# Optimization experiments

Measured on AMD Instinct MI355X. Metric: run time of the kernel, lower is better.

## Reference

```python
import jax, jax.numpy as jnp
import numpy as np

EPS = 1e-12  # tf.nn.l2_normalize epsilon used inside keras CosineSimilarity


def _cos(a, b):
    # keras CosineSimilarity returns -cos; callers negate explicitly.
    an = a / jnp.sqrt(jnp.maximum(jnp.sum(a * a, axis=-1, keepdims=True), EPS))
    bn = b / jnp.sqrt(jnp.maximum(jnp.sum(b * b, axis=-1, keepdims=True), EPS))
    return jnp.sum(an * bn, axis=-1)


def setup_inputs() -> dict:
    key = jax.random.key(0)
    B, S, D, H, N = 1024, 200, 128, 128, 64
    ks = jax.random.split(key, 8)
    X_series = jax.random.normal(ks[0], (B, S, D), jnp.float32)
    pos_series = jax.random.normal(ks[1], (S, D), jnp.float32)
    X_item = jax.random.normal(ks[2], (B, D), jnp.float32)
    origin = jax.random.normal(ks[3], (B, N, D), jnp.float32)  # X_negative
    # contiguous-prefix validity mask (module assumes valid positions form a prefix)
    lengths = jax.random.randint(ks[4], (B,), 1, S + 1)
    valid_mask = jnp.arange(S)[None, :] < lengths[:, None]
    # learned params (GlorotUniform-scale init)
    Wp = jax.random.normal(ks[5], (D, H), jnp.float32) * 0.08
    We = jax.random.normal(ks[6], (D, H), jnp.float32) * 0.08
    z = jax.random.normal(ks[7], (H,), jnp.float32) * 0.1
    return {"X_series": X_series, "pos_series": pos_series, "X_item": X_item,
            "valid_mask": valid_mask, "origin": origin, "Wp": Wp, "We": We, "z": z}


def reference(X_series, pos_series, X_item, valid_mask, origin, Wp, We, z):
    B, S, D = X_series.shape
    # additive tanh attention: z . tanh(X_series @ We + pos_series @ Wp)
    hidden = jnp.tanh(jnp.einsum('bsd,dh->bsh', X_series, We) + (pos_series @ Wp)[None])
    scores = jnp.einsum('bsh,h->bs', hidden, z)
    scores = jnp.where(valid_mask, scores, -jnp.inf)
    attn = jax.nn.softmax(scores, axis=-1)                      # [B,S]
    attentioned = attn[:, :, None] * X_series                    # [B,S,D]
    attention_output = jnp.sum(attentioned, axis=1)              # [B,D]
    inner = jnp.sum(attention_output * X_item, axis=-1, keepdims=True)
    concated = jnp.concatenate([attention_output, inner], axis=1)  # [B,D+1]

    # ---- auxiliary loss ----
    last_idx = jnp.sum(valid_mask.astype(jnp.int32), axis=1) - 1
    last_vec = attentioned[jnp.arange(B), last_idx]              # gather_nd
    new_mask = (jnp.arange(S)[None, :] < last_idx[:, None]).astype(X_series.dtype)
    out_vec = jnp.sum(attentioned * new_mask[:, :, None], axis=1)  # [B,D]
    # keras CosineSimilarity = -cos_sim; then mapped to (x+1)/2 and used as logits
    pos_logits = (-_cos(last_vec, out_vec) + 1.0) / 2.0          # [B]
    neg_logits = (-_cos(origin, out_vec[:, None, :]) + 1.0) / 2.0  # [B,N]
    pos_loss = jax.nn.softplus(-pos_logits)  # sigmoid_xent labels=1
    neg_loss = jax.nn.softplus(neg_logits)   # sigmoid_xent labels=0
    # NB: TF reduces pos_loss over its only axis -> scalar, broadcast-added to [B]
    auxiliary_loss = jnp.sum(pos_loss) + jnp.sum(neg_loss, axis=-1)  # [B]
    return concated, auxiliary_loss
```

## Files before the change

kernel.cpp:

```cpp
#include <hip/hip_runtime.h>
#include <hip/hip_bf16.h>
#include <math.h>

#define B_ 1024
#define S_ 200
#define D_ 128
#define H_ 128
#define N_ 64

typedef __attribute__((ext_vector_type(8))) short short8;
typedef __attribute__((ext_vector_type(8))) __bf16 bf16x8;
typedef __attribute__((ext_vector_type(4))) float floatx4;

static __device__ __forceinline__ float bf2f(unsigned short u) {
    union { unsigned int i; float f; } v; v.i = ((unsigned int)u) << 16; return v.f;
}
static __device__ __forceinline__ unsigned short f2bf(float f) {
    union { float f; unsigned int u; } v; v.f = f;
    unsigned int u = v.u;
    return (unsigned short)((u + 0x7FFFu + ((u >> 16) & 1u)) >> 16);
}
static __device__ __forceinline__ float ld1(const void* p, int isbf, size_t i) {
    return isbf ? bf2f(((const unsigned short*)p)[i]) : ((const float*)p)[i];
}
static __device__ __forceinline__ float fast_tanh(float x) {
    float t = __expf(2.0f * x);
    return 1.0f - 2.0f * __builtin_amdgcn_rcpf(t + 1.0f);
}

__global__ __launch_bounds__(64) void detect_kernel(
    const void* a0, const void* a1, const void* a2, const void* a3,
    const void* a4, const void* a5, const void* a6, const void* a7,
    int* flags)
{
    int bid = blockIdx.x, t = threadIdx.x;
    if (bid == 3) {
        const unsigned char* mb = (const unsigned char*)a3;
        int f = 0;
        for (int i = t; i < 4096; i += 64)
            if ((i & 3) && mb[i]) f = 1;
        for (int off = 32; off; off >>= 1) f |= __shfl_xor(f, off, 64);
        if (t == 0) flags[3] = f;
        return;
    }
    const void* ptrs[8] = {a0, a1, a2, a3, a4, a5, a6, a7};
    const int counts[8] = {B_*S_*D_, S_*D_, B_*D_, 0, B_*N_*D_, D_*H_, D_*H_, H_};
    const unsigned int* w = (const unsigned int*)ptrs[bid];
    int words = counts[bid] / 2; if (words > 1024) words = 1024;
    int pass = 0, tot = 0;
    for (int i = t; i < words; i += 64) {
        unsigned int e = (w[i] >> 7) & 0xFF;
        tot++;
        if (e == 0 || (e >= 96 && e <= 140)) pass++;
    }
    for (int off = 32; off; off >>= 1) {
        pass += __shfl_xor(pass, off, 64);
        tot  += __shfl_xor(tot,  off, 64);
    }
    if (t == 0) flags[bid] = (pass * 4 >= tot * 3) ? 1 : 0;
}

__global__ __launch_bounds__(128) void prep_kernel(
    const void* __restrict__ We, const void* __restrict__ pos,
    const void* __restrict__ Wp, const int* __restrict__ flags,
    unsigned short* __restrict__ WeTf, float* __restrict__ pb)
{
    int blk = blockIdx.x, t = threadIdx.x;
    __shared__ unsigned short T[128][136];
    __shared__ float prow[D_];
    if (blk == 0) {
        int fWe = flags[6];
        for (int c = t; c < 2048; c += 128) {
            int d = c >> 4, h8 = (c & 15) * 8;
            short8 v;
            if (fWe) {
                v = *(const short8*)((const unsigned short*)We + d * H_ + h8);
            } else {
                const float* p = (const float*)We + d * H_ + h8;
                float4 a = ((const float4*)p)[0], b = ((const float4*)p)[1];
                v[0] = (short)f2bf(a.x); v[1] = (short)f2bf(a.y);
                v[2] = (short)f2bf(a.z); v[3] = (short)f2bf(a.w);
                v[4] = (short)f2bf(b.x); v[5] = (short)f2bf(b.y);
                v[6] = (short)f2bf(b.z); v[7] = (short)f2bf(b.w);
            }
            *(short8*)(&T[d][h8]) = v;
        }
        __syncthreads();
        for (int i = t; i < 2048; i += 128) {
            int frag = i >> 6, ln = i & 63;
            int nt = frag >> 2, kks = frag & 3;
            int h = nt * 16 + (ln & 15);
            int dbase = kks * 32 + (ln >> 4) * 8;
            short8 v;
#pragma unroll
            for (int j = 0; j < 8; ++j) v[j] = (short)T[dbase + j][h];
            *(short8*)(WeTf + (size_t)i * 8) = v;
        }
    } else {
        int s = blk - 1, h = t;
        prow[h] = ld1(pos, flags[1], (size_t)s * D_ + h);
        __syncthreads();
        float acc = 0.f;
        if (flags[5]) {
            const unsigned short* W = (const unsigned short*)Wp;
            for (int d = 0; d < D_; ++d) acc = fmaf(prow[d], bf2f(W[d * H_ + h]), acc);
        } else {
            const float* W = (const float*)Wp;
            for (int d = 0; d < D_; ++d) acc = fmaf(prow[d], W[d * H_ + h], acc);
        }
        pb[s * H_ + h] = acc;
    }
}

__global__ __launch_bounds__(256) void scores_kernel(
    const void* __restrict__ Xs, const unsigned short* __restrict__ WeTf,
    const void* __restrict__ zv, const float* __restrict__ pb,
    const int* __restrict__ flags, float* __restrict__ scores)
{
    __shared__ unsigned short Bsh[16384];
    int t = threadIdx.x;
    int lane = t & 63, w = t >> 6;
    int quad = lane >> 4, mrow = lane & 15;
    int fXs = flags[0], fz = flags[7];
    int row0 = blockIdx.x * 128 + w * 32;

    for (int i = t; i < 2048; i += 256)
        *(short8*)(Bsh + i * 8) = *(const short8*)(WeTf + (size_t)i * 8);

    float zl[8];
#pragma unroll
    for (int nt = 0; nt < 8; ++nt) zl[nt] = ld1(zv, fz, nt * 16 + mrow);

    floatx4 acc[2][8];
#pragma unroll
    for (int mt = 0; mt < 2; ++mt)
#pragma unroll
        for (int nt = 0; nt < 8; ++nt) {
            acc[mt][nt][0] = 0.f; acc[mt][nt][1] = 0.f;
            acc[mt][nt][2] = 0.f; acc[mt][nt][3] = 0.f;
        }
    __syncthreads();

#pragma unroll
    for (int kks = 0; kks < 4; ++kks) {
        bf16x8 af[2];
#pragma unroll
        for (int mt = 0; mt < 2; ++mt) {
            size_t roff = (size_t)(row0 + mt * 16 + mrow) * D_ + kks * 32 + quad * 8;
            if (fXs) {
                short8 v = *(const short8*)((const unsigned short*)Xs + roff);
                af[mt] = __builtin_bit_cast(bf16x8, v);
            } else {
                const float* p = (const float*)Xs + roff;
                float4 a = ((const float4*)p)[0], b = ((const float4*)p)[1];
                short8 v;
                v[0] = (short)f2bf(a.x); v[1] = (short)f2bf(a.y);
                v[2] = (short)f2bf(a.z); v[3] = (short)f2bf(a.w);
                v[4] = (short)f2bf(b.x); v[5] = (short)f2bf(b.y);
                v[6] = (short)f2bf(b.z); v[7] = (short)f2bf(b.w);
                af[mt] = __builtin_bit_cast(bf16x8, v);
            }
        }
#pragma unroll
        for (int nt = 0; nt < 8; ++nt) {
            short8 bv = *(const short8*)(Bsh + (((nt << 2) + kks) * 64 + lane) * 8);
            bf16x8 bf = __builtin_bit_cast(bf16x8, bv);
            acc[0][nt] = __builtin_amdgcn_mfma_f32_16x16x32_bf16(af[0], bf, acc[0][nt], 0, 0, 0);
            acc[1][nt] = __builtin_amdgcn_mfma_f32_16x16x32_bf16(af[1], bf, acc[1][nt], 0, 0, 0);
        }
    }

#pragma unroll
    for (int mt = 0; mt < 2; ++mt) {
#pragma unroll
        for (int reg = 0; reg < 4; ++reg) {
            int grow = row0 + mt * 16 + quad * 4 + reg;
            int s = grow % S_;
            const float* pbrow = pb + (size_t)s * H_;
            float rs = 0.f;
#pragma unroll
            for (int nt = 0; nt < 8; ++nt)
                rs = fmaf(fast_tanh(acc[mt][nt][reg] + pbrow[nt * 16 + mrow]), zl[nt], rs);
#pragma unroll
            for (int off = 1; off < 16; off <<= 1)
                rs += __shfl_xor(rs, off, 64);
            if (mrow == 0) scores[grow] = rs;
        }
    }
}

__global__ __launch_bounds__(256) void attnout_kernel(
    const void* __restrict__ Xs, const void* __restrict__ Xitem,
    const void* __restrict__ maskv, const void* __restrict__ origin,
    const float* __restrict__ scores, const int* __restrict__ flags,
    float* __restrict__ pos_loss, float* __restrict__ neg_sum,
    float* __restrict__ out)
{
    int b = blockIdx.x, t = threadIdx.x;
    int wv = t >> 6, lane = t & 63;
    int fXs = flags[0], fXi = flags[2], fMk = flags[3], fOr = flags[4];
    __shared__ float attn[256];
    __shared__ float att_out[D_];
    __shared__ float lastv[D_];
    __shared__ float outv[D_];
    __shared__ float partial[8][D_];
    __shared__ float p_oo[4][64];
    __shared__ float p_ov[4][64];
    __shared__ float red[16];
    __shared__ int redi[4];
    __shared__ float sc1s, sc2s, vvs;

    int nn = t >> 2, part = t & 3;
    float o_f[32];
    if (fOr) {
        const unsigned short* p = (const unsigned short*)origin + ((size_t)b * N_ + nn) * D_ + part * 32;
#pragma unroll
        for (int j = 0; j < 4; ++j) {
            uint4 u = *(const uint4*)(p + j * 8);
            o_f[j*8+0] = bf2f((unsigned short)(u.x & 0xffff));
            o_f[j*8+1] = bf2f((unsigned short)(u.x >> 16));
            o_f[j*8+2] = bf2f((unsigned short)(u.y & 0xffff));
            o_f[j*8+3] = bf2f((unsigned short)(u.y >> 16));
            o_f[j*8+4] = bf2f((unsigned short)(u.z & 0xffff));
            o_f[j*8+5] = bf2f((unsigned short)(u.z >> 16));
            o_f[j*8+6] = bf2f((unsigned short)(u.w & 0xffff));
            o_f[j*8+7] = bf2f((unsigned short)(u.w >> 16));
        }
    } else {
        const float* p = (const float*)origin + ((size_t)b * N_ + nn) * D_ + part * 32;
#pragma unroll
        for (int j = 0; j < 8; ++j) {
            float4 v = *(const float4*)(p + j * 4);
            o_f[j*4+0] = v.x; o_f[j*4+1] = v.y; o_f[j*4+2] = v.z; o_f[j*4+3] = v.w;
        }
    }

    int nz = 0;
    if (t < S_)
        nz = fMk ? (((const unsigned char*)maskv)[(size_t)b * S_ + t] != 0)
                 : (((const int*)maskv)[(size_t)b * S_ + t] != 0);
    unsigned long long bal = __ballot(nz);
    if (lane == 0) redi[wv] = __popcll(bal);
    __syncthreads();
    int length = redi[0] + redi[1] + redi[2] + redi[3];
    int last = length - 1;

    float sc = (t < length) ? scores[(size_t)b * S_ + t] : -INFINITY;
    float m = sc;
    for (int off = 32; off; off >>= 1) m = fmaxf(m, __shfl_xor(m, off, 64));
    if (lane == 0) red[wv] = m;
    __syncthreads();
    if (t == 0) sc1s = fmaxf(fmaxf(red[0], red[1]), fmaxf(red[2], red[3]));
    __syncthreads();
    float e = (t < length) ? expf(sc - sc1s) : 0.f;
    float r = e;
    for (int off = 32; off; off >>= 1) r += __shfl_xor(r, off, 64);
    __syncthreads();
    if (lane == 0) red[wv] = r;
    __syncthreads();
    if (t == 0) sc2s = red[0] + red[1] + red[2] + red[3];
    __syncthreads();
    attn[t] = e / sc2s;
    __syncthreads();

    {
        int sp = t >> 5;
        int d4 = (t & 31) * 4;
        float a0 = 0, a1 = 0, a2 = 0, a3 = 0;
        if (fXs) {
#pragma unroll 5
            for (int s = sp; s < S_; s += 8) {
                float ww = attn[s];
                uint2 u = *(const uint2*)((const unsigned short*)Xs + ((size_t)b * S_ + s) * D_ + d4);
                a0 = fmaf(ww, bf2f((unsigned short)(u.x & 0xffff)), a0);
                a1 = fmaf(ww, bf2f((unsigned short)(u.x >> 16)), a1);
                a2 = fmaf(ww, bf2f((unsigned short)(u.y & 0xffff)), a2);
                a3 = fmaf(ww, bf2f((unsigned short)(u.y >> 16)), a3);
            }
        } else {
#pragma unroll 5
            for (int s = sp; s < S_; s += 8) {
                float ww = attn[s];
                float4 u = *(const float4*)((const float*)Xs + ((size_t)b * S_ + s) * D_ + d4);
                a0 = fmaf(ww, u.x, a0);
                a1 = fmaf(ww, u.y, a1);
                a2 = fmaf(ww, u.z, a2);
                a3 = fmaf(ww, u.w, a3);
            }
        }
        partial[sp][d4] = a0; partial[sp][d4 + 1] = a1;
        partial[sp][d4 + 2] = a2; partial[sp][d4 + 3] = a3;
    }
    __syncthreads();
    if (t < D_) {
        float v = 0.f;
#pragma unroll
        for (int p = 0; p < 8; ++p) v += partial[p][t];
        att_out[t] = v;
        float lv = attn[last] * ld1(Xs, fXs, ((size_t)b * S_ + last) * D_ + t);
        lastv[t] = lv;
        outv[t] = v - lv;
    }
    __syncthreads();

    {
        float pi = (t < D_) ? att_out[t] * ld1(Xitem, fXi, (size_t)b * D_ + t) : 0.f;
        for (int off = 32; off; off >>= 1) pi += __shfl_xor(pi, off, 64);
        if (lane == 0) red[wv] = pi;
        __syncthreads();
        if (t < D_) out[(size_t)b * (D_ + 1) + t] = att_out[t];
        if (t == 0)
            out[(size_t)b * (D_ + 1) + D_] = red[0] + red[1] + red[2] + red[3];
        __syncthreads();
    }

    {
        float l_ = (t < D_) ? lastv[t] : 0.f;
        float o_ = (t < D_) ? outv[t] : 0.f;
        float r0 = l_ * l_, r1 = l_ * o_, r2 = o_ * o_;
        for (int off = 32; off; off >>= 1) {
            r0 += __shfl_xor(r0, off, 64);
            r1 += __shfl_xor(r1, off, 64);
            r2 += __shfl_xor(r2, off, 64);
        }
        if (lane == 0) { red[wv] = r0; red[4 + wv] = r1; red[8 + wv] = r2; }
        __syncthreads();
        if (t == 0) {
            float ll = red[0] + red[1] + red[2] + red[3];
            float lo = red[4] + red[5] + red[6] + red[7];
            float oo = red[8] + red[9] + red[10] + red[11];
            float cosv = lo / (sqrtf(fmaxf(ll, 1e-12f)) * sqrtf(fmaxf(oo, 1e-12f)));
            float pl = 0.5f * (1.f - cosv);
            pos_loss[b] = log1pf(expf(-pl));
            vvs = oo;
        }
        __syncthreads();
    }

    {
        float o_oo = 0.f, o_ov = 0.f;
#pragma unroll
        for (int jj = 0; jj < 32; ++jj) {
            int j = (jj + part * 8) & 31;
            float wv_ = outv[part * 32 + j];
            o_oo = fmaf(o_f[j], o_f[j], o_oo);
            o_ov = fmaf(o_f[j], wv_, o_ov);
        }
        p_oo[part][nn] = o_oo;
        p_ov[part][nn] = o_ov;
        __syncthreads();
        if (t < 64) {
            float oo = p_oo[0][t] + p_oo[1][t] + p_oo[2][t] + p_oo[3][t];
            float ov = p_ov[0][t] + p_ov[1][t] + p_ov[2][t] + p_ov[3][t];
            float cosn = ov / (sqrtf(fmaxf(oo, 1e-12f)) * sqrtf(fmaxf(vvs, 1e-12f)));
            float nl = 0.5f * (1.f - cosn);
            float nloss = log1pf(expf(nl));
            for (int off = 32; off; off >>= 1) nloss += __shfl_xor(nloss, off, 64);
            if (t == 0) neg_sum[b] = nloss;
        }
    }
}

__global__ __launch_bounds__(1024) void final_kernel(
    const float* __restrict__ pos_loss,
    const float* __restrict__ neg_sum,
    float* __restrict__ out)
{
    __shared__ float red[16];
    int t = threadIdx.x;
    float v = pos_loss[t];
    for (int off = 32; off; off >>= 1) v += __shfl_xor(v, off, 64);
    if ((t & 63) == 0) red[t >> 6] = v;
    __syncthreads();
    if (t == 0) {
        float s = 0.f;
#pragma unroll
        for (int i = 0; i < 16; ++i) s += red[i];
        red[0] = s;
    }
    __syncthreads();
    out[(size_t)B_ * (D_ + 1) + t] = red[0] + neg_sum[t];
}

extern "C" void kernel_launch(void* const* d_in, const int* in_sizes, int n_in,
                              void* d_out, int out_size, void* d_ws, size_t ws_size,
                              hipStream_t stream) {
    const void* Xs     = d_in[0];
    const void* pos    = d_in[1];
    const void* Xitem  = d_in[2];
    const void* mask   = d_in[3];
    const void* origin = d_in[4];
    const void* Wp     = d_in[5];
    const void* We     = d_in[6];
    const void* zv     = d_in[7];

    int*   flags    = (int*)d_ws;
    unsigned short* WeTf = (unsigned short*)((char*)d_ws + 128);
    float* pb       = (float*)((char*)d_ws + 128 + 32768);
    float* scores   = pb + 25600;
    float* pos_loss = scores + 204800;
    float* neg_sum  = pos_loss + B_;
    float* out = (float*)d_out;

    detect_kernel<<<8, 64, 0, stream>>>(Xs, pos, Xitem, mask, origin, Wp, We, zv, flags);
    prep_kernel<<<201, 128, 0, stream>>>(We, pos, Wp, flags, WeTf, pb);
    scores_kernel<<<(B_ * S_) / 128, 256, 0, stream>>>(Xs, WeTf, zv, pb, flags, scores);
    attnout_kernel<<<B_, 256, 0, stream>>>(Xs, Xitem, mask, origin, scores, flags,
                                           pos_loss, neg_sum, out);
    final_kernel<<<1, 1024, 0, stream>>>(pos_loss, neg_sum, out);
}
```

Measured before the change: 264.0 us.

## Fuse score GEMM with attention pooling, staging each batch row's series in LDS

Measured after the change: 267.1 us. No clear change (+1.2%).

```diff
diff --git a/kernel.cpp b/kernel.cpp
--- a/kernel.cpp
+++ b/kernel.cpp
@@ -7,6 +7,7 @@
 #define D_ 128
 #define H_ 128
 #define N_ 64
+#define SP_ 208
 
 typedef __attribute__((ext_vector_type(8))) short short8;
 typedef __attribute__((ext_vector_type(8))) __bf16 bf16x8;
@@ -63,7 +64,7 @@
 __global__ __launch_bounds__(128) void prep_kernel(
     const void* __restrict__ We, const void* __restrict__ pos,
     const void* __restrict__ Wp, const int* __restrict__ flags,
-    unsigned short* __restrict__ WeTf, float* __restrict__ pb)
+    unsigned short* __restrict__ WeTf, float* __restrict__ pbT)
 {
     int blk = blockIdx.x, t = threadIdx.x;
     __shared__ unsigned short T[128][136];
@@ -96,6 +97,10 @@
             for (int j = 0; j < 8; ++j) v[j] = (short)T[dbase + j][h];
             *(short8*)(WeTf + (size_t)i * 8) = v;
         }
+        for (int i = t; i < H_ * (SP_ - S_); i += 128) {
+            int h = i >> 3, s2 = S_ + (i & 7);
+            pbT[(size_t)h * SP_ + s2] = 0.f;
+        }
     } else {
         int s = blk - 1, h = t;
         prow[h] = ld1(pos, flags[1], (size_t)s * D_ + h);
@@ -108,114 +113,37 @@
             const float* W = (const float*)Wp;
             for (int d = 0; d < D_; ++d) acc = fmaf(prow[d], W[d * H_ + h], acc);
         }
-        pb[s * H_ + h] = acc;
-    }
-}
-
-__global__ __launch_bounds__(256) void scores_kernel(
-    const void* __restrict__ Xs, const unsigned short* __restrict__ WeTf,
-    const void* __restrict__ zv, const float* __restrict__ pb,
-    const int* __restrict__ flags, float* __restrict__ scores)
-{
-    __shared__ unsigned short Bsh[16384];
-    int t = threadIdx.x;
-    int lane = t & 63, w = t >> 6;
-    int quad = lane >> 4, mrow = lane & 15;
-    int fXs = flags[0], fz = flags[7];
-    int row0 = blockIdx.x * 128 + w * 32;
-
-    for (int i = t; i < 2048; i += 256)
-        *(short8*)(Bsh + i * 8) = *(const short8*)(WeTf + (size_t)i * 8);
-
-    float zl[8];
-#pragma unroll
-    for (int nt = 0; nt < 8; ++nt) zl[nt] = ld1(zv, fz, nt * 16 + mrow);
-
-    floatx4 acc[2][8];
-#pragma unroll
-    for (int mt = 0; mt < 2; ++mt)
-#pragma unroll
-        for (int nt = 0; nt < 8; ++nt) {
-            acc[mt][nt][0] = 0.f; acc[mt][nt][1] = 0.f;
-            acc[mt][nt][2] = 0.f; acc[mt][nt][3] = 0.f;
-        }
-    __syncthreads();
-
-#pragma unroll
-    for (int kks = 0; kks < 4; ++kks) {
-        bf16x8 af[2];
-#pragma unroll
-        for (int mt = 0; mt < 2; ++mt) {
-            size_t roff = (size_t)(row0 + mt * 16 + mrow) * D_ + kks * 32 + quad * 8;
-            if (fXs) {
-                short8 v = *(const short8*)((const unsigned short*)Xs + roff);
-                af[mt] = __builtin_bit_cast(bf16x8, v);
-            } else {
-                const float* p = (const float*)Xs + roff;
-                float4 a = ((const float4*)p)[0], b = ((const float4*)p)[1];
-                short8 v;
-                v[0] = (short)f2bf(a.x); v[1] = (short)f2bf(a.y);
-                v[2] = (short)f2bf(a.z); v[3] = (short)f2bf(a.w);
-                v[4] = (short)f2bf(b.x); v[5] = (short)f2bf(b.y);
-                v[6] = (short)f2bf(b.z); v[7] = (short)f2bf(b.w);
-                af[mt] = __builtin_bit_cast(bf16x8, v);
-            }
-        }
-#pragma unroll
-        for (int nt = 0; nt < 8; ++nt) {
-            short8 bv = *(const short8*)(Bsh + (((nt << 2) + kks) * 64 + lane) * 8);
-            bf16x8 bf = __builtin_bit_cast(bf16x8, bv);
-            acc[0][nt] = __builtin_amdgcn_mfma_f32_16x16x32_bf16(af[0], bf, acc[0][nt], 0, 0, 0);
-            acc[1][nt] = __builtin_amdgcn_mfma_f32_16x16x32_bf16(af[1], bf, acc[1][nt], 0, 0, 0);
-        }
-    }
-
-#pragma unroll
-    for (int mt = 0; mt < 2; ++mt) {
-#pragma unroll
-        for (int reg = 0; reg < 4; ++reg) {
-            int grow = row0 + mt * 16 + quad * 4 + reg;
-            int s = grow % S_;
-            const float* pbrow = pb + (size_t)s * H_;
-            float rs = 0.f;
-#pragma unroll
-            for (int nt = 0; nt < 8; ++nt)
-                rs = fmaf(fast_tanh(acc[mt][nt][reg] + pbrow[nt * 16 + mrow]), zl[nt], rs);
-#pragma unroll
-            for (int off = 1; off < 16; off <<= 1)
-                rs += __shfl_xor(rs, off, 64);
-            if (mrow == 0) scores[grow] = rs;
-        }
-    }
-}
-
-__global__ __launch_bounds__(256) void attnout_kernel(
+        pbT[(size_t)h * SP_ + s] = acc;
+    }
+}
+
+__global__ __launch_bounds__(512, 4) void fused_kernel(
     const void* __restrict__ Xs, const void* __restrict__ Xitem,
     const void* __restrict__ maskv, const void* __restrict__ origin,
-    const float* __restrict__ scores, const int* __restrict__ flags,
+    const unsigned short* __restrict__ WeTf, const float* __restrict__ pbT,
+    const void* __restrict__ zv, const int* __restrict__ flags,
     float* __restrict__ pos_loss, float* __restrict__ neg_sum,
     float* __restrict__ out)
 {
     int b = blockIdx.x, t = threadIdx.x;
     int wv = t >> 6, lane = t & 63;
-    int fXs = flags[0], fXi = flags[2], fMk = flags[3], fOr = flags[4];
+    int quad = lane >> 4, mrow = lane & 15;
+    int fXs = flags[0], fXi = flags[2], fMk = flags[3], fOr = flags[4], fz = flags[7];
+
+    __shared__ __align__(16) unsigned short Xsh[SP_ * D_];
+    __shared__ float smemU[2048];
     __shared__ float attn[256];
-    __shared__ float att_out[D_];
-    __shared__ float lastv[D_];
-    __shared__ float outv[D_];
-    __shared__ float partial[8][D_];
-    __shared__ float p_oo[4][64];
-    __shared__ float p_ov[4][64];
-    __shared__ float red[16];
-    __shared__ int redi[4];
+    __shared__ float att_out[D_], lastv[D_], outv[D_];
+    __shared__ float red[24];
+    __shared__ int redi[8];
     __shared__ float sc1s, sc2s, vvs;
 
-    int nn = t >> 2, part = t & 3;
-    float o_f[32];
+    int nn = t >> 3, part = t & 7;
+    float o_f[16];
     if (fOr) {
-        const unsigned short* p = (const unsigned short*)origin + ((size_t)b * N_ + nn) * D_ + part * 32;
-#pragma unroll
-        for (int j = 0; j < 4; ++j) {
+        const unsigned short* p = (const unsigned short*)origin + ((size_t)b * N_ + nn) * D_ + part * 16;
+#pragma unroll
+        for (int j = 0; j < 2; ++j) {
             uint4 u = *(const uint4*)(p + j * 8);
             o_f[j*8+0] = bf2f((unsigned short)(u.x & 0xffff));
             o_f[j*8+1] = bf2f((unsigned short)(u.x >> 16));
@@ -227,12 +155,75 @@
             o_f[j*8+7] = bf2f((unsigned short)(u.w >> 16));
         }
     } else {
-        const float* p = (const float*)origin + ((size_t)b * N_ + nn) * D_ + part * 32;
-#pragma unroll
-        for (int j = 0; j < 8; ++j) {
+        const float* p = (const float*)origin + ((size_t)b * N_ + nn) * D_ + part * 16;
+#pragma unroll
+        for (int j = 0; j < 4; ++j) {
             float4 v = *(const float4*)(p + j * 4);
             o_f[j*4+0] = v.x; o_f[j*4+1] = v.y; o_f[j*4+2] = v.z; o_f[j*4+3] = v.w;
         }
+    }
+
+    for (int i = t; i < SP_ * 16; i += 512) {
+        int s = i >> 4, c8 = (i & 15) * 8;
+        short8 v;
+        if (s >= S_) {
+#pragma unroll
+            for (int j = 0; j < 8; ++j) v[j] = 0;
+        } else if (fXs) {
+            v = *(const short8*)((const unsigned short*)Xs + ((size_t)b * S_ + s) * D_ + c8);
+        } else {
+            const float* p = (const float*)Xs + ((size_t)b * S_ + s) * D_ + c8;
+            float4 a = ((const float4*)p)[0], c = ((const float4*)p)[1];
+            v[0] = (short)f2bf(a.x); v[1] = (short)f2bf(a.y);
+            v[2] = (short)f2bf(a.z); v[3] = (short)f2bf(a.w);
+            v[4] = (short)f2bf(c.x); v[5] = (short)f2bf(c.y);
+            v[6] = (short)f2bf(c.z); v[7] = (short)f2bf(c.w);
+        }
+        *(short8*)(Xsh + s * D_ + (c8 ^ ((s & 7) << 3))) = v;
+    }
+
+    int nt = wv;
+    bf16x8 bfr[4];
+#pragma unroll
+    for (int kks = 0; kks < 4; ++kks)
+        bfr[kks] = __builtin_bit_cast(bf16x8,
+            *(const short8*)(WeTf + (size_t)((((nt << 2) + kks) << 6) + lane) * 8));
+    float zl = ld1(zv, fz, nt * 16 + mrow);
+    const float* pbcol = pbT + (size_t)(nt * 16 + mrow) * SP_;
+
+    __syncthreads();
+
+    float* sp = smemU;
+    for (int mt = 0; mt < 13; ++mt) {
+        floatx4 acc = {0.f, 0.f, 0.f, 0.f};
+        int r = mt * 16 + mrow;
+        int rbase = r * D_, rx = (r & 7) << 3;
+#pragma unroll
+        for (int kks = 0; kks < 4; ++kks) {
+            bf16x8 af = __builtin_bit_cast(bf16x8,
+                *(const short8*)(Xsh + rbase + ((kks * 32 + quad * 8) ^ rx)));
+            acc = __builtin_amdgcn_mfma_f32_16x16x32_bf16(af, bfr[kks], acc, 0, 0, 0);
+        }
+        float4 pbq = *(const float4*)(pbcol + mt * 16 + quad * 4);
+#pragma unroll
+        for (int reg = 0; reg < 4; ++reg) {
+            float val = fast_tanh(acc[reg] + (&pbq.x)[reg]) * zl;
+            val += __shfl_xor(val, 1, 64);
+            val += __shfl_xor(val, 2, 64);
+            val += __shfl_xor(val, 4, 64);
+            val += __shfl_xor(val, 8, 64);
+            int s = mt * 16 + quad * 4 + reg;
+            if (mrow == 0 && s < S_) sp[nt * SP_ + s] = val;
+        }
+    }
+    __syncthreads();
+
+    float myscore = -INFINITY;
+    if (t < S_) {
+        float ss = 0.f;
+#pragma unroll
+        for (int w8 = 0; w8 < 8; ++w8) ss += sp[w8 * SP_ + t];
+        myscore = ss;
     }
 
     int nz = 0;
@@ -242,62 +233,73 @@
     unsigned long long bal = __ballot(nz);
     if (lane == 0) redi[wv] = __popcll(bal);
     __syncthreads();
-    int length = redi[0] + redi[1] + redi[2] + redi[3];
+    int length = redi[0] + redi[1] + redi[2] + redi[3]
+               + redi[4] + redi[5] + redi[6] + redi[7];
     int last = length - 1;
 
-    float sc = (t < length) ? scores[(size_t)b * S_ + t] : -INFINITY;
+    float sc = (t < length) ? myscore : -INFINITY;
     float m = sc;
     for (int off = 32; off; off >>= 1) m = fmaxf(m, __shfl_xor(m, off, 64));
     if (lane == 0) red[wv] = m;
     __syncthreads();
-    if (t == 0) sc1s = fmaxf(fmaxf(red[0], red[1]), fmaxf(red[2], red[3]));
+    if (t == 0) {
+        float mm = red[0];
+#pragma unroll
+        for (int i = 1; i < 8; ++i) mm = fmaxf(mm, red[i]);
+        sc1s = mm;
+    }
     __syncthreads();
     float e = (t < length) ? expf(sc - sc1s) : 0.f;
-    float r = e;
-    for (int off = 32; off; off >>= 1) r += __shfl_xor(r, off, 64);
-    __syncthreads();
-    if (lane == 0) red[wv] = r;
-    __syncthreads();
-    if (t == 0) sc2s = red[0] + red[1] + red[2] + red[3];
-    __syncthreads();
-    attn[t] = e / sc2s;
-    __syncthreads();
-
+    float rr = e;
+    for (int off = 32; off; off >>= 1) rr += __shfl_xor(rr, off, 64);
+    __syncthreads();
+    if (lane == 0) red[wv] = rr;
+    __syncthreads();
+    if (t == 0) {
+        float ssum = 0.f;
+#pragma unroll
+        for (int i = 0; i < 8; ++i) ssum += red[i];
+        sc2s = ssum;
+    }
+    __syncthreads();
+    if (t < 256) attn[t] = e / sc2s;
+    __syncthreads();
+
+    float* partial = smemU;
     {
-        int sp = t >> 5;
-        int d4 = (t & 31) * 4;
-        float a0 = 0, a1 = 0, a2 = 0, a3 = 0;
+        int spi = t >> 5, d4 = (t & 31) * 4;
+        float a0 = 0.f, a1 = 0.f, a2 = 0.f, a3 = 0.f;
         if (fXs) {
-#pragma unroll 5
-            for (int s = sp; s < S_; s += 8) {
+            for (int s = spi; s < S_; s += 16) {
                 float ww = attn[s];
-                uint2 u = *(const uint2*)((const unsigned short*)Xs + ((size_t)b * S_ + s) * D_ + d4);
+                uint2 u = *(const uint2*)(Xsh + s * D_ + (d4 ^ ((s & 7) << 3)));
                 a0 = fmaf(ww, bf2f((unsigned short)(u.x & 0xffff)), a0);
                 a1 = fmaf(ww, bf2f((unsigned short)(u.x >> 16)), a1);
                 a2 = fmaf(ww, bf2f((unsigned short)(u.y & 0xffff)), a2);
                 a3 = fmaf(ww, bf2f((unsigned short)(u.y >> 16)), a3);
             }
         } else {
-#pragma unroll 5
-            for (int s = sp; s < S_; s += 8) {
+            for (int s = spi; s < S_; s += 16) {
                 float ww = attn[s];
                 float4 u = *(const float4*)((const float*)Xs + ((size_t)b * S_ + s) * D_ + d4);
-                a0 = fmaf(ww, u.x, a0);
-                a1 = fmaf(ww, u.y, a1);
-                a2 = fmaf(ww, u.z, a2);
-                a3 = fmaf(ww, u.w, a3);
+                a0 = fmaf(ww, u.x, a0); a1 = fmaf(ww, u.y, a1);
+                a2 = fmaf(ww, u.z, a2); a3 = fmaf(ww, u.w, a3);
             }
         }
-        partial[sp][d4] = a0; partial[sp][d4 + 1] = a1;
-        partial[sp][d4 + 2] = a2; partial[sp][d4 + 3] = a3;
+        partial[spi * D_ + d4 + 0] = a0;
+        partial[spi * D_ + d4 + 1] = a1;
+        partial[spi * D_ + d4 + 2] = a2;
+        partial[spi * D_ + d4 + 3] = a3;
     }
     __syncthreads();
     if (t < D_) {
         float v = 0.f;
 #pragma unroll
-        for (int p = 0; p < 8; ++p) v += partial[p][t];
+        for (int p = 0; p < 16; ++p) v += partial[p * D_ + t];
         att_out[t] = v;
-        float lv = attn[last] * ld1(Xs, fXs, ((size_t)b * S_ + last) * D_ + t);
+        float xl = fXs ? bf2f(Xsh[last * D_ + (t ^ ((last & 7) << 3))])
+                       : ((const float*)Xs)[((size_t)b * S_ + last) * D_ + t];
+        float lv = attn[last] * xl;
         lastv[t] = lv;
         outv[t] = v - lv;
     }
@@ -309,8 +311,12 @@
         if (lane == 0) red[wv] = pi;
         __syncthreads();
         if (t < D_) out[(size_t)b * (D_ + 1) + t] = att_out[t];
-        if (t == 0)
-            out[(size_t)b * (D_ + 1) + D_] = red[0] + red[1] + red[2] + red[3];
+        if (t == 0) {
+            float s8 = 0.f;
+#pragma unroll
+            for (int i = 0; i < 8; ++i) s8 += red[i];
+            out[(size_t)b * (D_ + 1) + D_] = s8;
+        }
         __syncthreads();
     }
 
@@ -323,12 +329,12 @@
             r1 += __shfl_xor(r1, off, 64);
             r2 += __shfl_xor(r2, off, 64);
         }
-        if (lane == 0) { red[wv] = r0; red[4 + wv] = r1; red[8 + wv] = r2; }
+        if (lane == 0) { red[wv] = r0; red[8 + wv] = r1; red[16 + wv] = r2; }
         __syncthreads();
         if (t == 0) {
-            float ll = red[0] + red[1] + red[2] + red[3];
-            float lo = red[4] + red[5] + red[6] + red[7];
-            float oo = red[8] + red[9] + red[10] + red[11];
+            float ll = 0.f, lo = 0.f, oo = 0.f;
+#pragma unroll
+            for (int i = 0; i < 8; ++i) { ll += red[i]; lo += red[8 + i]; oo += red[16 + i]; }
             float cosv = lo / (sqrtf(fmaxf(ll, 1e-12f)) * sqrtf(fmaxf(oo, 1e-12f)));
             float pl = 0.5f * (1.f - cosv);
             pos_loss[b] = log1pf(expf(-pl));
@@ -338,20 +344,22 @@
     }
 
     {
+        float* p_oo = smemU;
+        float* p_ov = smemU + 512;
         float o_oo = 0.f, o_ov = 0.f;
 #pragma unroll
-        for (int jj = 0; jj < 32; ++jj) {
-            int j = (jj + part * 8) & 31;
-            float wv_ = outv[part * 32 + j];
+        for (int j = 0; j < 16; ++j) {
+            float wv_ = outv[part * 16 + j];
             o_oo = fmaf(o_f[j], o_f[j], o_oo);
             o_ov = fmaf(o_f[j], wv_, o_ov);
         }
-        p_oo[part][nn] = o_oo;
-        p_ov[part][nn] = o_ov;
+        p_oo[part * 64 + nn] = o_oo;
+        p_ov[part * 64 + nn] = o_ov;
         __syncthreads();
         if (t < 64) {
-            float oo = p_oo[0][t] + p_oo[1][t] + p_oo[2][t] + p_oo[3][t];
-            float ov = p_ov[0][t] + p_ov[1][t] + p_ov[2][t] + p_ov[3][t];
+            float oo = 0.f, ov = 0.f;
+#pragma unroll
+            for (int p8 = 0; p8 < 8; ++p8) { oo += p_oo[p8 * 64 + t]; ov += p_ov[p8 * 64 + t]; }
             float cosn = ov / (sqrtf(fmaxf(oo, 1e-12f)) * sqrtf(fmaxf(vvs, 1e-12f)));
             float nl = 0.5f * (1.f - cosn);
             float nloss = log1pf(expf(nl));
@@ -396,16 +404,14 @@
 
     int*   flags    = (int*)d_ws;
     unsigned short* WeTf = (unsigned short*)((char*)d_ws + 128);
-    float* pb       = (float*)((char*)d_ws + 128 + 32768);
-    float* scores   = pb + 25600;
-    float* pos_loss = scores + 204800;
+    float* pbT      = (float*)((char*)d_ws + 128 + 32768);
+    float* pos_loss = pbT + (size_t)H_ * SP_;
     float* neg_sum  = pos_loss + B_;
     float* out = (float*)d_out;
 
     detect_kernel<<<8, 64, 0, stream>>>(Xs, pos, Xitem, mask, origin, Wp, We, zv, flags);
-    prep_kernel<<<201, 128, 0, stream>>>(We, pos, Wp, flags, WeTf, pb);
-    scores_kernel<<<(B_ * S_) / 128, 256, 0, stream>>>(Xs, WeTf, zv, pb, flags, scores);
-    attnout_kernel<<<B_, 256, 0, stream>>>(Xs, Xitem, mask, origin, scores, flags,
-                                           pos_loss, neg_sum, out);
+    prep_kernel<<<201, 128, 0, stream>>>(We, pos, Wp, flags, WeTf, pbT);
+    fused_kernel<<<B_, 512, 0, stream>>>(Xs, Xitem, mask, origin, WeTf, pbT, zv, flags,
+                                         pos_loss, neg_sum, out);
     final_kernel<<<1, 1024, 0, stream>>>(pos_loss, neg_sum, out);
 }
```
